# Optimization experiments

Measured on AMD Instinct MI355X. Metric: run time of the kernel, lower is better.

## Reference

```python
import jax, jax.numpy as jnp
import numpy as np

DIM = 1024
HEADS = 16
SCALE = DIM ** (-0.5)  # NOTE: module scales by full dim, not head_dim


def setup_inputs() -> dict:
    key = jax.random.key(0)
    k1, k2, k3, k4 = jax.random.split(key, 4)
    x = jax.random.normal(k1, (4, 2048, DIM), dtype=jnp.float32)
    # torch Linear weights: y = x @ W.T
    w_qkv = jax.random.normal(k2, (3 * DIM, DIM), dtype=jnp.float32) * (DIM ** -0.5)
    w_out = jax.random.normal(k3, (DIM, DIM), dtype=jnp.float32) * (DIM ** -0.5)
    b_out = jax.random.normal(k4, (DIM,), dtype=jnp.float32) * 0.01
    return {"x": x, "w_qkv": w_qkv, "w_out": w_out, "b_out": b_out}


def reference(x, w_qkv, w_out, b_out):
    b, n, _ = x.shape
    h = HEADS
    d = DIM // h
    qkv = x @ w_qkv.T                                   # [b, n, 3*dim]
    qkv = qkv.reshape(b, n, 3, h, d)                    # split (qkv h d)
    qkv = jnp.transpose(qkv, (2, 0, 3, 1, 4))           # [3, b, h, n, d]
    q, k, v = qkv[0], qkv[1], qkv[2]
    dots = jnp.einsum('bhid,bhjd->bhij', q, k) * SCALE  # [b, h, n, n]
    attn = jax.nn.softmax(dots, axis=-1)
    out = jnp.einsum('bhij,bhjd->bhid', attn, v)        # [b, h, n, d]
    out = jnp.transpose(out, (0, 2, 1, 3)).reshape(b, n, h * d)
    return out @ w_out.T + b_out
```

## Files before the change

### kernel.cpp

```cpp
#include <hip/hip_runtime.h>

typedef short bf16x8 __attribute__((ext_vector_type(8)));
typedef float f32x4 __attribute__((ext_vector_type(4)));
typedef float f32x16 __attribute__((ext_vector_type(16)));

static __device__ __forceinline__ unsigned short f2bf(float f) {
  union { float f; unsigned u; } v; v.f = f;
  unsigned r = v.u + 0x7fffu + ((v.u >> 16) & 1u);
  return (unsigned short)(r >> 16);
}

static __device__ __forceinline__ unsigned pk2bf(float lo, float hi) {
  union { float f; unsigned u; } a, b; a.f = lo; b.f = hi;
  unsigned ra = a.u + 0x7fffu + ((a.u >> 16) & 1u);
  unsigned rb = b.u + 0x7fffu + ((b.u >> 16) & 1u);
  return __builtin_amdgcn_perm(rb, ra, 0x07060302);
}

static __device__ __forceinline__ void gll16(const unsigned short* g,
                                             unsigned short* l) {
  __builtin_amdgcn_global_load_lds(
      (const __attribute__((address_space(1))) unsigned int*)g,
      (__attribute__((address_space(3))) unsigned int*)l, 16, 0, 0);
}

__global__ void cvt_kernel(const float* __restrict__ src,
                           unsigned short* __restrict__ dst, int n4) {
  int i = blockIdx.x * blockDim.x + threadIdx.x;
  if (i >= n4) return;
  float4 f = ((const float4*)src)[i];
  ushort4 o;
  o.x = f2bf(f.x); o.y = f2bf(f.y); o.z = f2bf(f.z); o.w = f2bf(f.w);
  ((ushort4*)dst)[i] = o;
}

#define TM 128
#define TN 128
#define BK 64

template <int EPI>
__global__ __launch_bounds__(256, 2)
void gemm_bt(const unsigned short* __restrict__ X,
             const unsigned short* __restrict__ W,
             unsigned short* __restrict__ QKV, float* __restrict__ OUT,
             const float* __restrict__ bias, int M, int N, int K) {
  __shared__ __align__(16) unsigned short As[TM * BK];
  __shared__ __align__(16) unsigned short Bs[TN * BK];

  const int tid = threadIdx.x;
  const int lane = tid & 63;
  const int wave = tid >> 6;
  const int quad = lane >> 4;
  const int l16 = lane & 15;
  const int wm = wave >> 1, wn = wave & 1;

  const int m0 = blockIdx.y * TM;
  const int n0 = blockIdx.x * TN;

  const int sr = lane >> 3, sc = (lane & 7) * 8;

  f32x4 zero = {0.f, 0.f, 0.f, 0.f};
  f32x4 acc[4][4];
#pragma unroll
  for (int i = 0; i < 4; i++)
#pragma unroll
    for (int j = 0; j < 4; j++) acc[i][j] = zero;

  for (int k0 = 0; k0 < K; k0 += BK) {
    __syncthreads();
#pragma unroll
    for (int c = 0; c < 4; c++) {
      int row = wave * 32 + c * 8;
      gll16(&X[(size_t)(m0 + row + sr) * K + k0 + sc], &As[row * BK]);
      gll16(&W[(size_t)(n0 + row + sr) * K + k0 + sc], &Bs[row * BK]);
    }
    __syncthreads();
#pragma unroll
    for (int kk = 0; kk < 2; kk++) {
      bf16x8 af[4], bfr[4];
#pragma unroll
      for (int t = 0; t < 4; t++) {
        af[t]  = *(const bf16x8*)&As[(wm * 64 + t * 16 + l16) * BK + kk * 32 + quad * 8];
        bfr[t] = *(const bf16x8*)&Bs[(wn * 64 + t * 16 + l16) * BK + kk * 32 + quad * 8];
      }
#pragma unroll
      for (int mt = 0; mt < 4; mt++)
#pragma unroll
        for (int nt = 0; nt < 4; nt++)
          acc[mt][nt] = __builtin_amdgcn_mfma_f32_16x16x32_bf16(
              af[mt], bfr[nt], acc[mt][nt], 0, 0, 0);
    }
  }

#pragma unroll
  for (int mt = 0; mt < 4; mt++) {
#pragma unroll
    for (int nt = 0; nt < 4; nt++) {
      if (EPI == 0) {
        int nbase = n0 + wn * 64 + nt * 16;
        int which = nbase >> 10;
        if (which == 2) {
          int rem = (nbase + l16) & 1023;
          int h = rem >> 6, dd = rem & 63;
          int growb = m0 + wm * 64 + mt * 16 + quad * 4;
          int b = growb >> 11, nn0 = growb & 2047;
          ushort4 o;
          o.x = f2bf(acc[mt][nt][0]);
          o.y = f2bf(acc[mt][nt][1]);
          o.z = f2bf(acc[mt][nt][2]);
          o.w = f2bf(acc[mt][nt][3]);
          *(ushort4*)&QKV[16777216u + (((size_t)(b * 16 + h) * 64 + dd) << 11) + nn0] = o;
        } else {
#pragma unroll
          for (int r = 0; r < 4; r++) {
            int grow = m0 + wm * 64 + mt * 16 + quad * 4 + r;
            int gcol = nbase + l16;
            int rem = gcol & 1023;
            int h = rem >> 6, dd = rem & 63;
            float v = acc[mt][nt][r];
            if (which == 0) v *= 0.04508422f;
            int b = grow >> 11, nn = grow & 2047;
            QKV[(size_t)which * 8388608 +
                ((size_t)(b * 16 + h) * 2048 + nn) * 64 + dd] = f2bf(v);
          }
        }
      } else {
#pragma unroll
        for (int r = 0; r < 4; r++) {
          int grow = m0 + wm * 64 + mt * 16 + quad * 4 + r;
          int gcol = n0 + wn * 64 + nt * 16 + l16;
          OUT[(size_t)grow * N + gcol] = acc[mt][nt][r] + bias[gcol];
        }
      }
    }
  }
}

#define SK 72

__global__ __launch_bounds__(256, 2)
void attn_kernel(const unsigned short* __restrict__ Qg,
                 const unsigned short* __restrict__ Kg,
                 const unsigned short* __restrict__ Vg,
                 unsigned short* __restrict__ AO) {
  __shared__ __align__(16) unsigned short K_s[64 * SK];
  __shared__ __align__(16) unsigned short V_s[64 * SK];

  const int tid = threadIdx.x;
  const int lane = tid & 63;
  const int wave = tid >> 6;
  const int l31 = lane & 31;
  const int hh = lane >> 5;

  const int qb = blockIdx.x;
  const int bh = blockIdx.y;
  const size_t base = (size_t)bh * 131072;
  const int q0 = qb * 256 + wave * 64;

  bf16x8 bq[2][4];
#pragma unroll
  for (int mt = 0; mt < 2; mt++)
#pragma unroll
    for (int ks = 0; ks < 4; ks++)
      bq[mt][ks] = *(const bf16x8*)&Qg[base + (size_t)(q0 + mt * 32 + l31) * 64 +
                                       ks * 16 + hh * 8];

  f32x16 O[2][2];
#pragma unroll
  for (int mt = 0; mt < 2; mt++)
#pragma unroll
    for (int dt = 0; dt < 2; dt++)
#pragma unroll
      for (int r = 0; r < 16; r++) O[mt][dt][r] = 0.f;
  float lrow[2] = {0.f, 0.f};

  const int s_r = tid >> 3;
  const int s_c = (tid & 7) * 8;

  for (int j0 = 0; j0 < 2048; j0 += 64) {
    __syncthreads();
    *(uint4*)&K_s[s_r * SK + s_c] =
        *(const uint4*)&Kg[base + (size_t)(j0 + s_r) * 64 + s_c];
    *(uint4*)&K_s[(s_r + 32) * SK + s_c] =
        *(const uint4*)&Kg[base + (size_t)(j0 + s_r + 32) * 64 + s_c];
    *(uint4*)&V_s[s_r * SK + s_c] =
        *(const uint4*)&Vg[base + (size_t)s_r * 2048 + j0 + s_c];
    *(uint4*)&V_s[(s_r + 32) * SK + s_c] =
        *(const uint4*)&Vg[base + (size_t)(s_r + 32) * 2048 + j0 + s_c];
    __syncthreads();

    f32x16 S[2][2];
#pragma unroll
    for (int sub = 0; sub < 2; sub++) {
      f32x16 a0, a1;
#pragma unroll
      for (int r = 0; r < 16; r++) { a0[r] = 0.f; a1[r] = 0.f; }
#pragma unroll
      for (int ks = 0; ks < 4; ks++) {
        bf16x8 kf = *(const bf16x8*)&K_s[(sub * 32 + l31) * SK + ks * 16 + hh * 8];
        a0 = __builtin_amdgcn_mfma_f32_32x32x16_bf16(kf, bq[0][ks], a0, 0, 0, 0);
        a1 = __builtin_amdgcn_mfma_f32_32x32x16_bf16(kf, bq[1][ks], a1, 0, 0, 0);
      }
      S[sub][0] = a0; S[sub][1] = a1;
    }

#pragma unroll
    for (int mt = 0; mt < 2; mt++) {
      float rsum = 0.f;
#pragma unroll
      for (int sub = 0; sub < 2; sub++)
#pragma unroll
        for (int r = 0; r < 16; r++) {
          float p = __builtin_amdgcn_exp2f(S[sub][mt][r]);
          S[sub][mt][r] = p;
          rsum += p;
        }
      lrow[mt] += rsum;
    }

#pragma unroll
    for (int win = 0; win < 4; win++) {
      const int sub = win >> 1, kk = win & 1;
      const int g0 = kk * 2, g1 = kk * 2 + 1;
      bf16x8 pf[2];
#pragma unroll
      for (int mt = 0; mt < 2; mt++) {
        unsigned a00 = pk2bf(S[sub][mt][4 * g0 + 0], S[sub][mt][4 * g0 + 1]);
        unsigned a01 = pk2bf(S[sub][mt][4 * g0 + 2], S[sub][mt][4 * g0 + 3]);
        unsigned a10 = pk2bf(S[sub][mt][4 * g1 + 0], S[sub][mt][4 * g1 + 1]);
        unsigned a11 = pk2bf(S[sub][mt][4 * g1 + 2], S[sub][mt][4 * g1 + 3]);
        unsigned b00 = __shfl_xor((int)a00, 32);
        unsigned b01 = __shfl_xor((int)a01, 32);
        unsigned b10 = __shfl_xor((int)a10, 32);
        unsigned b11 = __shfl_xor((int)a11, 32);
        union { unsigned u[4]; bf16x8 v; } fr;
        fr.u[0] = hh ? b10 : a00;
        fr.u[1] = hh ? b11 : a01;
        fr.u[2] = hh ? a10 : b00;
        fr.u[3] = hh ? a11 : b01;
        pf[mt] = fr.v;
      }
#pragma unroll
      for (int dt = 0; dt < 2; dt++) {
        bf16x8 vf = *(const bf16x8*)&V_s[(dt * 32 + l31) * SK + win * 16 + hh * 8];
#pragma unroll
        for (int mt = 0; mt < 2; mt++)
          O[mt][dt] = __builtin_amdgcn_mfma_f32_32x32x16_bf16(vf, pf[mt], O[mt][dt], 0, 0, 0);
      }
    }
  }

  const int b4 = bh >> 4, head = bh & 15;
#pragma unroll
  for (int mt = 0; mt < 2; mt++) {
    lrow[mt] += __shfl_xor(lrow[mt], 32);
    float inv = 1.0f / lrow[mt];
    int row = b4 * 2048 + q0 + mt * 32 + l31;
#pragma unroll
    for (int dt = 0; dt < 2; dt++)
#pragma unroll
      for (int g = 0; g < 4; g++) {
        ushort4 o;
        o.x = f2bf(O[mt][dt][4 * g + 0] * inv);
        o.y = f2bf(O[mt][dt][4 * g + 1] * inv);
        o.z = f2bf(O[mt][dt][4 * g + 2] * inv);
        o.w = f2bf(O[mt][dt][4 * g + 3] * inv);
        *(ushort4*)&AO[(size_t)row * 1024 + head * 64 + dt * 32 + 8 * g + 4 * hh] = o;
      }
  }
}

extern "C" void kernel_launch(void* const* d_in, const int* in_sizes, int n_in,
                              void* d_out, int out_size, void* d_ws,
                              size_t ws_size, hipStream_t stream) {
  const float* x     = (const float*)d_in[0];
  const float* w_qkv = (const float*)d_in[1];
  const float* w_out = (const float*)d_in[2];
  const float* b_out = (const float*)d_in[3];
  float* out = (float*)d_out;

  unsigned short* ws = (unsigned short*)d_ws;
  unsigned short* Xbf  = ws;
  unsigned short* Wqkv = ws + 8388608;
  unsigned short* Wout = ws + 11534336;
  unsigned short* QKV  = ws + 12582912;
  unsigned short* AO   = ws;

  cvt_kernel<<<8192, 256, 0, stream>>>(x, Xbf, 2097152);
  cvt_kernel<<<3072, 256, 0, stream>>>(w_qkv, Wqkv, 786432);
  cvt_kernel<<<1024, 256, 0, stream>>>(w_out, Wout, 262144);

  gemm_bt<0><<<dim3(3072 / TN, 8192 / TM), 256, 0, stream>>>(
      Xbf, Wqkv, QKV, nullptr, nullptr, 8192, 3072, 1024);

  attn_kernel<<<dim3(8, 64), 256, 0, stream>>>(
      QKV, QKV + 8388608, QKV + 16777216, AO);

  gemm_bt<1><<<dim3(1024 / TN, 8192 / TM), 256, 0, stream>>>(
      AO, Wout, nullptr, out, b_out, 8192, 1024, 1024);
}
```

Before: 288.3 us.

## Swizzle GEMM LDS, double-buffer attention K/V, fp16 PV path, fuse conversions

The GEMM's LDS tile layout is XOR-swizzled to avoid bank conflicts on MFMA fragment reads. The attention kernel double-buffers K/V in LDS with register prefetch, which removes one barrier per iteration and overlaps global loads with compute. V and P are now stored as fp16, P is packed with cvt_pkrtz, and the half-wave exchange uses permlane32_swap when available, all feeding an f16 MFMA. The three input-conversion launches are merged into one kernel. Switching to fp16 for V and P changes rounding and overflow behaviour but keeps the precision width the same.

```diff
diff --git a/kernel.cpp b/kernel.cpp
--- a/kernel.cpp
+++ b/kernel.cpp
@@ -1,8 +1,11 @@
 #include <hip/hip_runtime.h>
 
 typedef short bf16x8 __attribute__((ext_vector_type(8)));
+typedef _Float16 f16x8 __attribute__((ext_vector_type(8)));
+typedef __fp16 fp16x2 __attribute__((ext_vector_type(2)));
 typedef float f32x4 __attribute__((ext_vector_type(4)));
 typedef float f32x16 __attribute__((ext_vector_type(16)));
+typedef unsigned u32x2 __attribute__((ext_vector_type(2)));
 
 static __device__ __forceinline__ unsigned short f2bf(float f) {
   union { float f; unsigned u; } v; v.f = f;
@@ -10,11 +13,14 @@
   return (unsigned short)(r >> 16);
 }
 
-static __device__ __forceinline__ unsigned pk2bf(float lo, float hi) {
-  union { float f; unsigned u; } a, b; a.f = lo; b.f = hi;
-  unsigned ra = a.u + 0x7fffu + ((a.u >> 16) & 1u);
-  unsigned rb = b.u + 0x7fffu + ((b.u >> 16) & 1u);
-  return __builtin_amdgcn_perm(rb, ra, 0x07060302);
+static __device__ __forceinline__ unsigned short f2h(float f) {
+  union { _Float16 h; unsigned short u; } c; c.h = (_Float16)f; return c.u;
+}
+
+static __device__ __forceinline__ unsigned pkh(float lo, float hi) {
+  union { fp16x2 h; unsigned u; } c;
+  c.h = __builtin_amdgcn_cvt_pkrtz(lo, hi);
+  return c.u;
 }
 
 static __device__ __forceinline__ void gll16(const unsigned short* g,
@@ -24,11 +30,16 @@
       (__attribute__((address_space(3))) unsigned int*)l, 16, 0, 0);
 }
 
-__global__ void cvt_kernel(const float* __restrict__ src,
-                           unsigned short* __restrict__ dst, int n4) {
+__global__ void cvt3_kernel(const float* __restrict__ a,
+                            const float* __restrict__ b,
+                            const float* __restrict__ c,
+                            unsigned short* __restrict__ dst) {
   int i = blockIdx.x * blockDim.x + threadIdx.x;
-  if (i >= n4) return;
-  float4 f = ((const float4*)src)[i];
+  const float* src; int off;
+  if (i < 2097152) { src = a; off = 0; }
+  else if (i < 2883584) { src = b; off = 2097152; }
+  else { src = c; off = 2883584; }
+  float4 f = ((const float4*)src)[i - off];
   ushort4 o;
   o.x = f2bf(f.x); o.y = f2bf(f.y); o.z = f2bf(f.z); o.w = f2bf(f.w);
   ((ushort4*)dst)[i] = o;
@@ -53,11 +64,13 @@
   const int quad = lane >> 4;
   const int l16 = lane & 15;
   const int wm = wave >> 1, wn = wave & 1;
+  const int rc = l16 & 7;
 
   const int m0 = blockIdx.y * TM;
   const int n0 = blockIdx.x * TN;
 
-  const int sr = lane >> 3, sc = (lane & 7) * 8;
+  const int sr = lane >> 3;
+  const int gsc = ((lane & 7) ^ sr) * 8;
 
   f32x4 zero = {0.f, 0.f, 0.f, 0.f};
   f32x4 acc[4][4];
@@ -71,17 +84,18 @@
 #pragma unroll
     for (int c = 0; c < 4; c++) {
       int row = wave * 32 + c * 8;
-      gll16(&X[(size_t)(m0 + row + sr) * K + k0 + sc], &As[row * BK]);
-      gll16(&W[(size_t)(n0 + row + sr) * K + k0 + sc], &Bs[row * BK]);
+      gll16(&X[(size_t)(m0 + row + sr) * K + k0 + gsc], &As[row * BK]);
+      gll16(&W[(size_t)(n0 + row + sr) * K + k0 + gsc], &Bs[row * BK]);
     }
     __syncthreads();
 #pragma unroll
     for (int kk = 0; kk < 2; kk++) {
       bf16x8 af[4], bfr[4];
+      const int csw = ((kk * 4 + quad) ^ rc) * 8;
 #pragma unroll
       for (int t = 0; t < 4; t++) {
-        af[t]  = *(const bf16x8*)&As[(wm * 64 + t * 16 + l16) * BK + kk * 32 + quad * 8];
-        bfr[t] = *(const bf16x8*)&Bs[(wn * 64 + t * 16 + l16) * BK + kk * 32 + quad * 8];
+        af[t]  = *(const bf16x8*)&As[(wm * 64 + t * 16 + l16) * BK + csw];
+        bfr[t] = *(const bf16x8*)&Bs[(wn * 64 + t * 16 + l16) * BK + csw];
       }
 #pragma unroll
       for (int mt = 0; mt < 4; mt++)
@@ -105,10 +119,10 @@
           int growb = m0 + wm * 64 + mt * 16 + quad * 4;
           int b = growb >> 11, nn0 = growb & 2047;
           ushort4 o;
-          o.x = f2bf(acc[mt][nt][0]);
-          o.y = f2bf(acc[mt][nt][1]);
-          o.z = f2bf(acc[mt][nt][2]);
-          o.w = f2bf(acc[mt][nt][3]);
+          o.x = f2h(acc[mt][nt][0]);
+          o.y = f2h(acc[mt][nt][1]);
+          o.z = f2h(acc[mt][nt][2]);
+          o.w = f2h(acc[mt][nt][3]);
           *(ushort4*)&QKV[16777216u + (((size_t)(b * 16 + h) * 64 + dd) << 11) + nn0] = o;
         } else {
 #pragma unroll
@@ -143,8 +157,8 @@
                  const unsigned short* __restrict__ Kg,
                  const unsigned short* __restrict__ Vg,
                  unsigned short* __restrict__ AO) {
-  __shared__ __align__(16) unsigned short K_s[64 * SK];
-  __shared__ __align__(16) unsigned short V_s[64 * SK];
+  __shared__ __align__(16) unsigned short K_s[2][64 * SK];
+  __shared__ __align__(16) unsigned short V_s[2][64 * SK];
 
   const int tid = threadIdx.x;
   const int lane = tid & 63;
@@ -174,20 +188,27 @@
       for (int r = 0; r < 16; r++) O[mt][dt][r] = 0.f;
   float lrow[2] = {0.f, 0.f};
 
-  const int s_r = tid >> 3;
-  const int s_c = (tid & 7) * 8;
-
-  for (int j0 = 0; j0 < 2048; j0 += 64) {
-    __syncthreads();
-    *(uint4*)&K_s[s_r * SK + s_c] =
-        *(const uint4*)&Kg[base + (size_t)(j0 + s_r) * 64 + s_c];
-    *(uint4*)&K_s[(s_r + 32) * SK + s_c] =
-        *(const uint4*)&Kg[base + (size_t)(j0 + s_r + 32) * 64 + s_c];
-    *(uint4*)&V_s[s_r * SK + s_c] =
-        *(const uint4*)&Vg[base + (size_t)s_r * 2048 + j0 + s_c];
-    *(uint4*)&V_s[(s_r + 32) * SK + s_c] =
-        *(const uint4*)&Vg[base + (size_t)(s_r + 32) * 2048 + j0 + s_c];
-    __syncthreads();
+  const int sr = lane >> 3, sc = (lane & 7) * 8;
+  const unsigned short* Kp = Kg + base + (size_t)(wave * 16 + sr) * 64 + sc;
+  const unsigned short* Vp = Vg + base + (size_t)(wave * 16 + sr) * 2048 + sc;
+  const int woff = (wave * 16 + sr) * SK + sc;
+
+  uint4 kr0, kr1, vr0, vr1;
+  kr0 = *(const uint4*)Kp;           kr1 = *(const uint4*)(Kp + 512);
+  vr0 = *(const uint4*)Vp;           vr1 = *(const uint4*)(Vp + 16384);
+  *(uint4*)&K_s[0][woff] = kr0;      *(uint4*)&K_s[0][woff + 8 * SK] = kr1;
+  *(uint4*)&V_s[0][woff] = vr0;      *(uint4*)&V_s[0][woff + 8 * SK] = vr1;
+  __syncthreads();
+
+  for (int t = 0; t < 32; t++) {
+    const unsigned short* Kc = K_s[t & 1];
+    const unsigned short* Vc = V_s[t & 1];
+    if (t < 31) {
+      const unsigned short* kp = Kp + (size_t)(t + 1) * 4096;
+      const unsigned short* vp = Vp + (size_t)(t + 1) * 64;
+      kr0 = *(const uint4*)kp;  kr1 = *(const uint4*)(kp + 512);
+      vr0 = *(const uint4*)vp;  vr1 = *(const uint4*)(vp + 16384);
+    }
 
     f32x16 S[2][2];
 #pragma unroll
@@ -197,7 +218,7 @@
       for (int r = 0; r < 16; r++) { a0[r] = 0.f; a1[r] = 0.f; }
 #pragma unroll
       for (int ks = 0; ks < 4; ks++) {
-        bf16x8 kf = *(const bf16x8*)&K_s[(sub * 32 + l31) * SK + ks * 16 + hh * 8];
+        bf16x8 kf = *(const bf16x8*)&Kc[(sub * 32 + l31) * SK + ks * 16 + hh * 8];
         a0 = __builtin_amdgcn_mfma_f32_32x32x16_bf16(kf, bq[0][ks], a0, 0, 0, 0);
         a1 = __builtin_amdgcn_mfma_f32_32x32x16_bf16(kf, bq[1][ks], a1, 0, 0, 0);
       }
@@ -222,32 +243,45 @@
     for (int win = 0; win < 4; win++) {
       const int sub = win >> 1, kk = win & 1;
       const int g0 = kk * 2, g1 = kk * 2 + 1;
-      bf16x8 pf[2];
+      f16x8 pf[2];
 #pragma unroll
       for (int mt = 0; mt < 2; mt++) {
-        unsigned a00 = pk2bf(S[sub][mt][4 * g0 + 0], S[sub][mt][4 * g0 + 1]);
-        unsigned a01 = pk2bf(S[sub][mt][4 * g0 + 2], S[sub][mt][4 * g0 + 3]);
-        unsigned a10 = pk2bf(S[sub][mt][4 * g1 + 0], S[sub][mt][4 * g1 + 1]);
-        unsigned a11 = pk2bf(S[sub][mt][4 * g1 + 2], S[sub][mt][4 * g1 + 3]);
+        unsigned a00 = pkh(S[sub][mt][4 * g0 + 0], S[sub][mt][4 * g0 + 1]);
+        unsigned a01 = pkh(S[sub][mt][4 * g0 + 2], S[sub][mt][4 * g0 + 3]);
+        unsigned a10 = pkh(S[sub][mt][4 * g1 + 0], S[sub][mt][4 * g1 + 1]);
+        unsigned a11 = pkh(S[sub][mt][4 * g1 + 2], S[sub][mt][4 * g1 + 3]);
+        union { unsigned u[4]; f16x8 v; } fr;
+#if __has_builtin(__builtin_amdgcn_permlane32_swap)
+        u32x2 r0 = __builtin_amdgcn_permlane32_swap(a00, a10, false, false);
+        u32x2 r1 = __builtin_amdgcn_permlane32_swap(a01, a11, false, false);
+        fr.u[0] = r0.x; fr.u[1] = r1.x; fr.u[2] = r0.y; fr.u[3] = r1.y;
+#else
         unsigned b00 = __shfl_xor((int)a00, 32);
         unsigned b01 = __shfl_xor((int)a01, 32);
         unsigned b10 = __shfl_xor((int)a10, 32);
         unsigned b11 = __shfl_xor((int)a11, 32);
-        union { unsigned u[4]; bf16x8 v; } fr;
         fr.u[0] = hh ? b10 : a00;
         fr.u[1] = hh ? b11 : a01;
         fr.u[2] = hh ? a10 : b00;
         fr.u[3] = hh ? a11 : b01;
+#endif
         pf[mt] = fr.v;
       }
 #pragma unroll
       for (int dt = 0; dt < 2; dt++) {
-        bf16x8 vf = *(const bf16x8*)&V_s[(dt * 32 + l31) * SK + win * 16 + hh * 8];
+        f16x8 vf = *(const f16x8*)&Vc[(dt * 32 + l31) * SK + win * 16 + hh * 8];
 #pragma unroll
         for (int mt = 0; mt < 2; mt++)
-          O[mt][dt] = __builtin_amdgcn_mfma_f32_32x32x16_bf16(vf, pf[mt], O[mt][dt], 0, 0, 0);
-      }
-    }
+          O[mt][dt] = __builtin_amdgcn_mfma_f32_32x32x16_f16(vf, pf[mt], O[mt][dt], 0, 0, 0);
+      }
+    }
+
+    if (t < 31) {
+      const int nb = (t + 1) & 1;
+      *(uint4*)&K_s[nb][woff] = kr0;  *(uint4*)&K_s[nb][woff + 8 * SK] = kr1;
+      *(uint4*)&V_s[nb][woff] = vr0;  *(uint4*)&V_s[nb][woff + 8 * SK] = vr1;
+    }
+    __syncthreads();
   }
 
   const int b4 = bh >> 4, head = bh & 15;
@@ -286,9 +320,7 @@
   unsigned short* QKV  = ws + 12582912;
   unsigned short* AO   = ws;
 
-  cvt_kernel<<<8192, 256, 0, stream>>>(x, Xbf, 2097152);
-  cvt_kernel<<<3072, 256, 0, stream>>>(w_qkv, Wqkv, 786432);
-  cvt_kernel<<<1024, 256, 0, stream>>>(w_out, Wout, 262144);
+  cvt3_kernel<<<12288, 256, 0, stream>>>(x, w_qkv, w_out, Xbf);
 
   gemm_bt<0><<<dim3(3072 / TN, 8192 / TM), 256, 0, stream>>>(
       Xbf, Wqkv, QKV, nullptr, nullptr, 8192, 3072, 1024);
```

Result: faster. 260.4 us (-9.7%).
